# Kernel tuning notes

Hardware: AMD Instinct MI355X
Metric: run time of the kernel (lower is better)

## Reference

```python
import jax, jax.numpy as jnp
import numpy as np

HEADS = 20
HEAD_DIM = 64
NUM_IP = 20          # num_content_tokens (4) + num_style_tokens (16)
FU_SCALE = 0.5
STYLE_SCALE = 1.0
SCALE = 1.0 / np.sqrt(HEAD_DIM).astype(np.float32)


def setup_inputs() -> dict:
    key = jax.random.key(0)
    ks = jax.random.split(key, 9)
    B, S, H, C = 4, 4096, 1280, 2048
    T = 77 + NUM_IP  # text tokens + ip tokens
    w = 0.02
    return {
        "hidden_states": jax.random.normal(ks[0], (B, S, H), jnp.float32),
        "encoder_hidden_states": jax.random.normal(ks[1], (B, T, C), jnp.float32),
        "Wq": jax.random.normal(ks[2], (H, H), jnp.float32) * w,
        "Wk": jax.random.normal(ks[3], (H, C), jnp.float32) * w,
        "Wv": jax.random.normal(ks[4], (H, C), jnp.float32) * w,
        "Wk_ip": jax.random.normal(ks[5], (H, C), jnp.float32) * w,
        "Wv_ip": jax.random.normal(ks[6], (H, C), jnp.float32) * w,
        "Wo": jax.random.normal(ks[7], (H, H), jnp.float32) * w,
        "bo": jnp.zeros((H,), jnp.float32),
    }


def _to_heads(x):
    # [B, T, H] -> [B, heads, T, head_dim]
    B, T, _ = x.shape
    return x.reshape(B, T, HEADS, HEAD_DIM).transpose(0, 2, 1, 3)


def _blend(p):
    # cross-batch prob fusion: rows 1<-0, 3<-2 (CFG pairs)
    p = p.at[1].set(FU_SCALE * p[1] + (1.0 - FU_SCALE) * p[0])
    p = p.at[3].set(FU_SCALE * p[3] + (1.0 - FU_SCALE) * p[2])
    return p


def reference(hidden_states, encoder_hidden_states, Wq, Wk, Wv, Wk_ip, Wv_ip, Wo, bo):
    B, S, H = hidden_states.shape
    text = encoder_hidden_states[:, :-NUM_IP, :]   # [B, 77, C]
    ip = encoder_hidden_states[:, -NUM_IP:, :]     # [B, 20, C]

    q = _to_heads(hidden_states @ Wq.T)            # [B, h, S, d]
    k = _to_heads(text @ Wk.T)                     # [B, h, 77, d]
    v = _to_heads(text @ Wv.T)

    # fuAttn branch: explicit probs, blended across batch, then PV matmul
    probs = jax.nn.softmax(jnp.einsum('bhqd,bhkd->bhqk', q, k) * SCALE, axis=-1)
    probs = _blend(probs)
    raw = jnp.einsum('bhqk,bhkd->bhqd', probs, v)
    raw = raw.transpose(0, 2, 1, 3).reshape(B, S, H)

    # IP-adapter style cross-attention (fuIPAttn branch)
    ip_k = _to_heads(ip @ Wk_ip.T)                 # [B, h, 20, d]
    ip_v = _to_heads(ip @ Wv_ip.T)
    ip_probs = jax.nn.softmax(jnp.einsum('bhqd,bhkd->bhqk', q, ip_k) * SCALE, axis=-1)
    ip_probs = _blend(ip_probs)
    ip_hs = jnp.einsum('bhqk,bhkd->bhqd', ip_probs, ip_v)
    ip_hs = ip_hs.transpose(0, 2, 1, 3).reshape(B, S, H)

    hs = raw + STYLE_SCALE * ip_hs
    # batch rows 0 and 2 keep raw (text-only) attention output
    hs = hs.at[0].set(raw[0]).at[2].set(raw[2])

    # to_out[0] linear (bias) + to_out[1] dropout (identity at inference)
    return hs @ Wo.T + bo
```

## Files before the change

kernel.cpp:

```cpp
#include <hip/hip_runtime.h>
#include <cstdint>

typedef float floatx4 __attribute__((ext_vector_type(4)));
typedef __bf16 bf16x8 __attribute__((ext_vector_type(8)));

typedef const __attribute__((address_space(1))) void* gas_cvp;
typedef __attribute__((address_space(3))) void* las_vp;

__device__ __forceinline__ float bflo(unsigned int u) {
    return __builtin_bit_cast(float, u << 16);
}
__device__ __forceinline__ float bfhi(unsigned int u) {
    return __builtin_bit_cast(float, u & 0xffff0000u);
}
__device__ __forceinline__ unsigned short f2bf(float f) {
    unsigned int u = __builtin_bit_cast(unsigned int, f);
    u += 0x7fffu + ((u >> 16) & 1u);
    return (unsigned short)(u >> 16);
}
__device__ __forceinline__ bf16x8 ld8(const unsigned short* p) {
    return __builtin_bit_cast(bf16x8, *(const uint4*)p);
}
__device__ __forceinline__ floatx4 mfma32(bf16x8 a, bf16x8 b, floatx4 c) {
    return __builtin_amdgcn_mfma_f32_16x16x32_bf16(a, b, c, 0, 0, 0);
}
__device__ __forceinline__ void load_lds16(const void* g, void* l) {
    __builtin_amdgcn_global_load_lds(
        (gas_cvp)(unsigned long long)g,
        (las_vp)(unsigned int)(unsigned long long)l,
        16, 0, 0);
}

__global__ void cvt_f32_bf16(const float* __restrict__ in,
                             unsigned short* __restrict__ out, int n4) {
    int i = blockIdx.x * 256 + threadIdx.x;
    if (i < n4) {
        float4 v = ((const float4*)in)[i];
        ushort4 o;
        o.x = f2bf(v.x); o.y = f2bf(v.y); o.z = f2bf(v.z); o.w = f2bf(v.w);
        ((ushort4*)out)[i] = o;
    }
}

struct CvtJob { const float* src; unsigned short* dst; int n4; };
struct CvtJobs { CvtJob j[7]; };

__global__ void cvt_multi(CvtJobs jobs) {
    CvtJob jb = jobs.j[blockIdx.y];
    int i = blockIdx.x * 256 + threadIdx.x;
    if (i < jb.n4) {
        float4 v = ((const float4*)jb.src)[i];
        ushort4 o;
        o.x = f2bf(v.x); o.y = f2bf(v.y); o.z = f2bf(v.z); o.w = f2bf(v.w);
        ((ushort4*)jb.dst)[i] = o;
    }
}

struct GemmJob {
    const unsigned short* A;
    const unsigned short* B;
    void* C;
    int M, N, K;
    int rpb, bstride, roff;
};
struct GemmArgs { GemmJob j[5]; };

template <bool F32OUT>
__global__ __launch_bounds__(256, 2) void gemm_bt(GemmArgs args,
                                                  const float* __restrict__ bias) {
    GemmJob jb = args.j[blockIdx.z];
    const int ntiles = jb.N >> 7;
    const int mtiles = (jb.M + 127) >> 7;

    int bx, by;
    {
        int idx = blockIdx.x;
        if ((mtiles & 7) == 0) {
            int gsz = ntiles * 8;
            int group = idx / gsz;
            int rem = idx - group * gsz;
            by = group * 8 + (rem & 7);
            bx = rem >> 3;
        } else {
            by = idx / ntiles;
            bx = idx - by * ntiles;
        }
    }
    if (by * 128 >= jb.M) return;

    const int tid  = threadIdx.x;
    const int lane = tid & 63;
    const int wid  = tid >> 6;
    const int K = jb.K, N = jb.N;

    __shared__ unsigned short ldsA[128 * 32];
    __shared__ unsigned short ldsB[128 * 32];

    const int colA = (((tid & 3) ^ ((tid >> 3) & 3)) * 8);
    auto maprow = [&](int r) -> size_t {
        r = (r < jb.M) ? r : (jb.M - 1);
        int b = r / jb.rpb;
        int t = r - b * jb.rpb;
        return (size_t)(b * jb.bstride + jb.roff + t);
    };
    const unsigned short* pa0 = jb.A + maprow(by * 128 + (tid >> 2)) * K + colA;
    const unsigned short* pa1 = jb.A + maprow(by * 128 + 64 + (tid >> 2)) * K + colA;
    const unsigned short* pb0 = jb.B + (size_t)(bx * 128 + (tid >> 2)) * K + colA;
    const unsigned short* pb1 = jb.B + (size_t)(bx * 128 + 64 + (tid >> 2)) * K + colA;

    unsigned short* la0 = &ldsA[tid * 8];
    unsigned short* la1 = &ldsA[2048 + tid * 8];
    unsigned short* lb0 = &ldsB[tid * 8];
    unsigned short* lb1 = &ldsB[2048 + tid * 8];

    floatx4 acc[4][4] = {};

    const int wm = (wid & 1) * 64;
    const int wn = (wid >> 1) * 64;
    const int fr = lane & 15;
    const int g  = lane >> 4;
    const int fcs = (g ^ ((fr >> 1) & 3)) * 8;

    for (int k0 = 0; k0 < K; k0 += 32) {
        __syncthreads();
        load_lds16(pa0 + k0, la0);
        load_lds16(pa1 + k0, la1);
        load_lds16(pb0 + k0, lb0);
        load_lds16(pb1 + k0, lb1);
        __syncthreads();

        bf16x8 af[4], bfv[4];
#pragma unroll
        for (int i = 0; i < 4; i++)
            af[i] = *(const bf16x8*)&ldsA[(wm + i * 16 + fr) * 32 + fcs];
#pragma unroll
        for (int i = 0; i < 4; i++)
            bfv[i] = *(const bf16x8*)&ldsB[(wn + i * 16 + fr) * 32 + fcs];
#pragma unroll
        for (int mi = 0; mi < 4; mi++)
#pragma unroll
            for (int ni = 0; ni < 4; ni++)
                acc[mi][ni] = __builtin_amdgcn_mfma_f32_16x16x32_bf16(
                    af[mi], bfv[ni], acc[mi][ni], 0, 0, 0);
    }

    const int colBase = bx * 128 + wn;
    const int rowBase = by * 128 + wm;
#pragma unroll
    for (int mi = 0; mi < 4; mi++) {
#pragma unroll
        for (int ni = 0; ni < 4; ni++) {
            int col  = colBase + ni * 16 + fr;
            int row0 = rowBase + mi * 16 + g * 4;
#pragma unroll
            for (int r = 0; r < 4; r++) {
                int row = row0 + r;
                if (row < jb.M) {
                    float v = acc[mi][ni][r];
                    if (F32OUT)
                        ((float*)jb.C)[(size_t)row * N + col] = v + bias[col];
                    else
                        ((unsigned short*)jb.C)[(size_t)row * N + col] = f2bf(v);
                }
            }
        }
    }
}

#define NT 77
#define NI 20
#define VSTR 104
#define ISTR 40

__global__ __launch_bounds__(256, 2) void attn_mfma(
    const unsigned short* __restrict__ q,
    const unsigned short* __restrict__ kt,
    const unsigned short* __restrict__ vt,
    const unsigned short* __restrict__ kip,
    const unsigned short* __restrict__ vip,
    unsigned short* __restrict__ outp)
{
    const int tid = threadIdx.x;
    const int qt = blockIdx.x;
    const int h  = blockIdx.y;
    const int pz = blockIdx.z;
    const int b0 = 2 * pz;
    const int lane  = tid & 63;
    const int w     = tid >> 6;
    const int bi    = w >> 1;
    const int strip = (w & 1) * 16;
    const int fr = lane & 15;
    const int g  = lane >> 4;

    __shared__ unsigned short sVt[2][64][VSTR];
    __shared__ unsigned short sVipt[2][64][ISTR];
    __shared__ unsigned short sP[2][32][VSTR];

    for (int i = tid; i < 2 * 64 * (VSTR - NT); i += 256) {
        int b = i / (64 * (VSTR - NT)); int rem = i % (64 * (VSTR - NT));
        sVt[b][rem / (VSTR - NT)][NT + rem % (VSTR - NT)] = 0;
    }
    for (int i = tid; i < 2 * 64 * (ISTR - NI); i += 256) {
        int b = i / (64 * (ISTR - NI)); int rem = i % (64 * (ISTR - NI));
        sVipt[b][rem / (ISTR - NI)][NI + rem % (ISTR - NI)] = 0;
    }
    for (int i = tid; i < 2 * 32 * (VSTR - 80); i += 256) {
        int b = i / (32 * (VSTR - 80)); int rem = i % (32 * (VSTR - 80));
        sP[b][rem / (VSTR - 80)][80 + rem % (VSTR - 80)] = 0;
    }

    for (int c = tid; c < 2 * 8 * NT; c += 256) {
        int b = c / (8 * NT); int rem = c % (8 * NT);
        int dc = rem / NT; int key = rem % NT;
        uint4 v = *(const uint4*)&vt[((size_t)((b0 + b) * NT + key)) * 1280 + h * 64 + dc * 8];
        unsigned int uu[4] = {v.x, v.y, v.z, v.w};
#pragma unroll
        for (int j = 0; j < 4; j++) {
            sVt[b][dc * 8 + 2 * j][key]     = (unsigned short)(uu[j] & 0xffffu);
            sVt[b][dc * 8 + 2 * j + 1][key] = (unsigned short)(uu[j] >> 16);
        }
    }
    for (int c = tid; c < 2 * 8 * NI; c += 256) {
        int b = c / (8 * NI); int rem = c % (8 * NI);
        int dc = rem / NI; int key = rem % NI;
        uint4 v = *(const uint4*)&vip[((size_t)((b0 + b) * NI + key)) * 1280 + h * 64 + dc * 8];
        unsigned int uu[4] = {v.x, v.y, v.z, v.w};
#pragma unroll
        for (int j = 0; j < 4; j++) {
            sVipt[b][dc * 8 + 2 * j][key]     = (unsigned short)(uu[j] & 0xffffu);
            sVipt[b][dc * 8 + 2 * j + 1][key] = (unsigned short)(uu[j] >> 16);
        }
    }

    const size_t qbase = ((size_t)((b0 + bi) * 4096 + qt * 32 + strip + fr)) * 1280 + h * 64;
    bf16x8 aq0 = ld8(&q[qbase + g * 8]);
    bf16x8 aq1 = ld8(&q[qbase + 32 + g * 8]);

    floatx4 sc[5] = {};
#pragma unroll
    for (int t = 0; t < 5; t++) {
        int key = t * 16 + fr; key = (key < NT) ? key : (NT - 1);
        const size_t kb = ((size_t)((b0 + bi) * NT + key)) * 1280 + h * 64;
        sc[t] = mfma32(aq0, ld8(&kt[kb + g * 8]), sc[t]);
        sc[t] = mfma32(aq1, ld8(&kt[kb + 32 + g * 8]), sc[t]);
    }

#pragma unroll
    for (int r = 0; r < 4; r++) {
        float m = -1e30f;
#pragma unroll
        for (int t = 0; t < 5; t++) {
            float v = sc[t][r] * 0.125f;
            if (t == 4 && fr >= 13) v = -1e30f;
            sc[t][r] = v;
            m = fmaxf(m, v);
        }
        m = fmaxf(m, __shfl_xor(m, 1));
        m = fmaxf(m, __shfl_xor(m, 2));
        m = fmaxf(m, __shfl_xor(m, 4));
        m = fmaxf(m, __shfl_xor(m, 8));
        float sum = 0.f;
#pragma unroll
        for (int t = 0; t < 5; t++) {
            float e = __expf(sc[t][r] - m);
            sc[t][r] = e;
            sum += e;
        }
        sum += __shfl_xor(sum, 1);
        sum += __shfl_xor(sum, 2);
        sum += __shfl_xor(sum, 4);
        sum += __shfl_xor(sum, 8);
        float inv = 1.f / sum;
#pragma unroll
        for (int t = 0; t < 5; t++)
            sP[bi][strip + g * 4 + r][t * 16 + fr] = f2bf(sc[t][r] * inv);
    }
    __syncthreads();

    {
        unsigned int* p0 = (unsigned int*)&sP[0][0][0];
        unsigned int* p1 = (unsigned int*)&sP[1][0][0];
        for (int i = tid; i < 32 * VSTR / 2; i += 256) {
            unsigned int a = p0[i], b = p1[i];
            unsigned short r0 = f2bf(0.5f * (bflo(a) + bflo(b)));
            unsigned short r1 = f2bf(0.5f * (bfhi(a) + bfhi(b)));
            p1[i] = (unsigned int)r0 | ((unsigned int)r1 << 16);
        }
    }
    __syncthreads();

    floatx4 accO[4] = {};
    {
        const unsigned short* prow = &sP[bi][strip + fr][0];
        bf16x8 pa0 = ld8(prow + g * 8);
        bf16x8 pa1 = ld8(prow + 32 + g * 8);
        bf16x8 pa2 = ld8(prow + 64 + g * 8);
#pragma unroll
        for (int dt = 0; dt < 4; dt++) {
            const unsigned short* vrow = &sVt[bi][dt * 16 + fr][0];
            accO[dt] = mfma32(pa0, ld8(vrow + g * 8), accO[dt]);
            accO[dt] = mfma32(pa1, ld8(vrow + 32 + g * 8), accO[dt]);
            accO[dt] = mfma32(pa2, ld8(vrow + 64 + g * 8), accO[dt]);
        }
    }

    floatx4 si[2] = {};
#pragma unroll
    for (int t = 0; t < 2; t++) {
        int key = t * 16 + fr; key = (key < NI) ? key : (NI - 1);
        const size_t kb = ((size_t)((b0 + bi) * NI + key)) * 1280 + h * 64;
        si[t] = mfma32(aq0, ld8(&kip[kb + g * 8]), si[t]);
        si[t] = mfma32(aq1, ld8(&kip[kb + 32 + g * 8]), si[t]);
    }
#pragma unroll
    for (int r = 0; r < 4; r++) {
        float v0 = si[0][r] * 0.125f;
        float v1 = (fr >= 4) ? -1e30f : si[1][r] * 0.125f;
        float m = fmaxf(v0, v1);
        m = fmaxf(m, __shfl_xor(m, 1));
        m = fmaxf(m, __shfl_xor(m, 2));
        m = fmaxf(m, __shfl_xor(m, 4));
        m = fmaxf(m, __shfl_xor(m, 8));
        float e0 = __expf(v0 - m), e1 = __expf(v1 - m);
        float s = e0 + e1;
        s += __shfl_xor(s, 1);
        s += __shfl_xor(s, 2);
        s += __shfl_xor(s, 4);
        s += __shfl_xor(s, 8);
        float inv = 1.f / s;
        si[0][r] = e0 * inv;
        si[1][r] = e1 * inv;
    }
    __syncthreads();

#pragma unroll
    for (int r = 0; r < 4; r++) {
        sP[bi][strip + g * 4 + r][fr]      = f2bf(si[0][r]);
        sP[bi][strip + g * 4 + r][16 + fr] = f2bf(si[1][r]);
    }
    __syncthreads();

    for (int i = tid; i < 32 * 16; i += 256) {
        int r = i >> 4, kk = i & 15;
        unsigned int* p0 = (unsigned int*)&sP[0][r][0];
        unsigned int* p1 = (unsigned int*)&sP[1][r][0];
        unsigned int a = p0[kk], b = p1[kk];
        unsigned short r0 = f2bf(0.5f * (bflo(a) + bflo(b)));
        unsigned short r1 = f2bf(0.5f * (bfhi(a) + bfhi(b)));
        p1[kk] = (unsigned int)r0 | ((unsigned int)r1 << 16);
    }
    __syncthreads();

    if (bi == 1) {
        const unsigned short* prow = &sP[1][strip + fr][0];
        bf16x8 pip = ld8(prow + g * 8);
#pragma unroll
        for (int dt = 0; dt < 4; dt++)
            accO[dt] = mfma32(pip, ld8(&sVipt[1][dt * 16 + fr][g * 8]), accO[dt]);
    }

    const size_t orow0 = (size_t)((b0 + bi) * 4096 + qt * 32 + strip);
#pragma unroll
    for (int dt = 0; dt < 4; dt++) {
        int col = h * 64 + dt * 16 + fr;
#pragma unroll
        for (int r = 0; r < 4; r++)
            outp[(orow0 + g * 4 + r) * 1280 + col] = f2bf(accO[dt][r]);
    }
}

extern "C" void kernel_launch(void* const* d_in, const int* in_sizes, int n_in,
                              void* d_out, int out_size, void* d_ws, size_t ws_size,
                              hipStream_t stream) {
    const float* hs   = (const float*)d_in[0];
    const float* ehs  = (const float*)d_in[1];
    const float* Wq   = (const float*)d_in[2];
    const float* Wk   = (const float*)d_in[3];
    const float* Wv   = (const float*)d_in[4];
    const float* Wkip = (const float*)d_in[5];
    const float* Wvip = (const float*)d_in[6];
    const float* Wo   = (const float*)d_in[7];
    const float* bo   = (const float*)d_in[8];

    char* w = (char*)d_ws;
    size_t off = 0;
    auto alloc = [&](size_t bytes) {
        char* pp = w + off;
        off += (bytes + 255) & ~(size_t)255;
        return pp;
    };
    unsigned short* hs_bf   = (unsigned short*)alloc(16384ull * 1280 * 2);
    unsigned short* q_bf    = (unsigned short*)alloc(16384ull * 1280 * 2);
    unsigned short* at_bf   = (unsigned short*)alloc(16384ull * 1280 * 2);
    unsigned short* ehs_bf  = (unsigned short*)alloc(4ull * 97 * 2048 * 2);
    unsigned short* Wq_bf   = (unsigned short*)alloc(1280ull * 1280 * 2);
    unsigned short* Wk_bf   = (unsigned short*)alloc(1280ull * 2048 * 2);
    unsigned short* Wv_bf   = (unsigned short*)alloc(1280ull * 2048 * 2);
    unsigned short* Wkip_bf = (unsigned short*)alloc(1280ull * 2048 * 2);
    unsigned short* Wvip_bf = (unsigned short*)alloc(1280ull * 2048 * 2);
    unsigned short* Wo_bf   = (unsigned short*)alloc(1280ull * 1280 * 2);
    unsigned short* kt  = (unsigned short*)alloc(308ull * 1280 * 2);
    unsigned short* vt  = (unsigned short*)alloc(308ull * 1280 * 2);
    unsigned short* kip = (unsigned short*)alloc(80ull * 1280 * 2);
    unsigned short* vip = (unsigned short*)alloc(80ull * 1280 * 2);

    cvt_f32_bf16<<<dim3(20480, 1, 1), 256, 0, stream>>>(hs, hs_bf, 16384 * 1280 / 4);

    CvtJobs cj{};
    cj.j[0] = CvtJob{ehs,  ehs_bf,  (int)(4ull * 97 * 2048 / 4)};
    cj.j[1] = CvtJob{Wq,   Wq_bf,   1280 * 1280 / 4};
    cj.j[2] = CvtJob{Wk,   Wk_bf,   1280 * 2048 / 4};
    cj.j[3] = CvtJob{Wv,   Wv_bf,   1280 * 2048 / 4};
    cj.j[4] = CvtJob{Wkip, Wkip_bf, 1280 * 2048 / 4};
    cj.j[5] = CvtJob{Wvip, Wvip_bf, 1280 * 2048 / 4};
    cj.j[6] = CvtJob{Wo,   Wo_bf,   1280 * 1280 / 4};
    cvt_multi<<<dim3(2560, 7, 1), 256, 0, stream>>>(cj);

    GemmArgs gq{};
    gq.j[0] = GemmJob{hs_bf,  Wq_bf,   (void*)q_bf, 16384, 1280, 1280, 16384, 0, 0};
    gq.j[1] = GemmJob{ehs_bf, Wk_bf,   (void*)kt,     308, 1280, 2048, 77, 97, 0};
    gq.j[2] = GemmJob{ehs_bf, Wv_bf,   (void*)vt,     308, 1280, 2048, 77, 97, 0};
    gq.j[3] = GemmJob{ehs_bf, Wkip_bf, (void*)kip,     80, 1280, 2048, 20, 97, 77};
    gq.j[4] = GemmJob{ehs_bf, Wvip_bf, (void*)vip,     80, 1280, 2048, 20, 97, 77};
    gemm_bt<false><<<dim3(1280, 1, 5), 256, 0, stream>>>(gq, nullptr);

    attn_mfma<<<dim3(128, 20, 2), 256, 0, stream>>>(q_bf, kt, vt, kip, vip, at_bf);

    GemmArgs go{};
    go.j[0] = GemmJob{at_bf, Wo_bf, d_out, 16384, 1280, 1280, 16384, 0, 0};
    gemm_bt<true><<<dim3(1280, 1, 1), 256, 0, stream>>>(go, bo);
}
```

Baseline: 453.4 us.

## Replace GEMM with 256x256-tile double-buffered pipelined kernel and flattened job grid

Rewrites the bf16 GEMM from 128x128 tiles with 256 threads and a single-stage LDS buffer into a 256x256-tile, 512-thread kernel. It uses a double-buffered 64-deep K loop that interleaves global-to-LDS prefetch with four MFMA phases, adds s_setprio and explicit vmcnt waits, and uses a swizzled LDS layout. The per-job launch with z-dimension and early exit is replaced by a flat block list with per-job start offsets, so the small K/V projections and the Q projection share one grid without idle blocks. The goal is higher MFMA utilization and more reuse per loaded byte. In exchange, N is hardcoded to 1280, LDS use is larger (128 KB per block), and the small-M jobs waste more of each 256-row tile.

```diff
diff --git a/kernel.cpp b/kernel.cpp
--- a/kernel.cpp
+++ b/kernel.cpp
@@ -56,111 +56,194 @@
     }
 }
 
-struct GemmJob {
+struct GJob {
     const unsigned short* A;
     const unsigned short* B;
     void* C;
-    int M, N, K;
+    int M, K;
     int rpb, bstride, roff;
+    int bstart;
 };
-struct GemmArgs { GemmJob j[5]; };
+struct GArgs { GJob j[5]; };
+
+#define GBAR() do { __builtin_amdgcn_s_barrier(); __builtin_amdgcn_sched_barrier(0); } while (0)
 
 template <bool F32OUT>
-__global__ __launch_bounds__(256, 2) void gemm_bt(GemmArgs args,
+__global__ __launch_bounds__(512, 2) void gemm256(GArgs args,
                                                   const float* __restrict__ bias) {
-    GemmJob jb = args.j[blockIdx.z];
-    const int ntiles = jb.N >> 7;
-    const int mtiles = (jb.M + 127) >> 7;
-
-    int bx, by;
+    const int tid = threadIdx.x;
+    int jid = 0;
+#pragma unroll
+    for (int t = 1; t < 5; ++t)
+        if ((int)blockIdx.x >= args.j[t].bstart) jid = t;
+    const GJob jb = args.j[jid];
+    const int K = jb.K;
+    int b = (int)blockIdx.x - jb.bstart;
     {
-        int idx = blockIdx.x;
-        if ((mtiles & 7) == 0) {
-            int gsz = ntiles * 8;
-            int group = idx / gsz;
-            int rem = idx - group * gsz;
-            by = group * 8 + (rem & 7);
-            bx = rem >> 3;
-        } else {
-            by = idx / ntiles;
-            bx = idx - by * ntiles;
-        }
-    }
-    if (by * 128 >= jb.M) return;
-
-    const int tid  = threadIdx.x;
-    const int lane = tid & 63;
-    const int wid  = tid >> 6;
-    const int K = jb.K, N = jb.N;
-
-    __shared__ unsigned short ldsA[128 * 32];
-    __shared__ unsigned short ldsB[128 * 32];
-
-    const int colA = (((tid & 3) ^ ((tid >> 3) & 3)) * 8);
+        const int mt = (jb.M + 255) >> 8;
+        const int nblk = mt * 5;
+        if ((nblk & 7) == 0) b = (b & 7) * (nblk >> 3) + (b >> 3);
+    }
+    const int by = b / 5, bx = b - by * 5;
+
+    __shared__ unsigned short ldsA[32768];
+    __shared__ unsigned short ldsB[32768];
+
+    const int srow   = ((tid >> 7) << 4) + ((tid >> 2) & 15);
+    const int schunk = ((tid & 3) << 4) ^ (((tid >> 2) & 6) << 3);
+    const int scol   = (((tid >> 6) & 1) << 5) + (schunk >> 1);
+
+    const int Mloc = jb.M, rpbL = jb.rpb, bstrL = jb.bstride, roffL = jb.roff;
     auto maprow = [&](int r) -> size_t {
-        r = (r < jb.M) ? r : (jb.M - 1);
-        int b = r / jb.rpb;
-        int t = r - b * jb.rpb;
-        return (size_t)(b * jb.bstride + jb.roff + t);
+        r = (r < Mloc) ? r : (Mloc - 1);
+        int blk = r / rpbL;
+        return (size_t)(blk * bstrL + roffL + (r - blk * rpbL));
     };
-    const unsigned short* pa0 = jb.A + maprow(by * 128 + (tid >> 2)) * K + colA;
-    const unsigned short* pa1 = jb.A + maprow(by * 128 + 64 + (tid >> 2)) * K + colA;
-    const unsigned short* pb0 = jb.B + (size_t)(bx * 128 + (tid >> 2)) * K + colA;
-    const unsigned short* pb1 = jb.B + (size_t)(bx * 128 + 64 + (tid >> 2)) * K + colA;
-
-    unsigned short* la0 = &ldsA[tid * 8];
-    unsigned short* la1 = &ldsA[2048 + tid * 8];
-    unsigned short* lb0 = &ldsB[tid * 8];
-    unsigned short* lb1 = &ldsB[2048 + tid * 8];
-
-    floatx4 acc[4][4] = {};
-
-    const int wm = (wid & 1) * 64;
-    const int wn = (wid >> 1) * 64;
-    const int fr = lane & 15;
-    const int g  = lane >> 4;
-    const int fcs = (g ^ ((fr >> 1) & 3)) * 8;
-
-    for (int k0 = 0; k0 < K; k0 += 32) {
-        __syncthreads();
-        load_lds16(pa0 + k0, la0);
-        load_lds16(pa1 + k0, la1);
-        load_lds16(pb0 + k0, lb0);
-        load_lds16(pb1 + k0, lb1);
-        __syncthreads();
-
-        bf16x8 af[4], bfv[4];
-#pragma unroll
-        for (int i = 0; i < 4; i++)
-            af[i] = *(const bf16x8*)&ldsA[(wm + i * 16 + fr) * 32 + fcs];
-#pragma unroll
-        for (int i = 0; i < 4; i++)
-            bfv[i] = *(const bf16x8*)&ldsB[(wn + i * 16 + fr) * 32 + fcs];
-#pragma unroll
-        for (int mi = 0; mi < 4; mi++)
-#pragma unroll
-            for (int ni = 0; ni < 4; ni++)
-                acc[mi][ni] = __builtin_amdgcn_mfma_f32_16x16x32_bf16(
-                    af[mi], bfv[ni], acc[mi][ni], 0, 0, 0);
-    }
-
-    const int colBase = bx * 128 + wn;
-    const int rowBase = by * 128 + wm;
-#pragma unroll
-    for (int mi = 0; mi < 4; mi++) {
-#pragma unroll
-        for (int ni = 0; ni < 4; ni++) {
-            int col  = colBase + ni * 16 + fr;
-            int row0 = rowBase + mi * 16 + g * 4;
-#pragma unroll
-            for (int r = 0; r < 4; r++) {
-                int row = row0 + r;
-                if (row < jb.M) {
-                    float v = acc[mi][ni][r];
+
+    const unsigned short* pA[2][2];
+    const unsigned short* pB[2][2];
+    unsigned short* dA[2][2];
+    unsigned short* dB[2][2];
+#pragma unroll
+    for (int h = 0; h < 2; ++h)
+#pragma unroll
+        for (int j = 0; j < 2; ++j) {
+            const int r = h * 128 + j * 64 + srow;
+            pA[h][j] = jb.A + maprow(by * 256 + r) * K + scol;
+            pB[h][j] = jb.B + (size_t)(bx * 256 + r) * K + scol;
+            dA[h][j] = &ldsA[h * 8192 + j * 4096 + tid * 8];
+            dB[h][j] = &ldsB[h * 8192 + j * 4096 + tid * 8];
+        }
+
+    const int lane = tid & 63, fr = lane & 15, g = lane >> 4;
+    const int w = tid >> 6, wr = w & 1, wc = w >> 1;
+    const int rb   = fr * 32 + ((g * 8) ^ ((fr & 6) << 2));
+    const int aoff = wr * 8192 + rb;
+    const int boff = (wc >> 1) * 8192 + (wc & 1) * 4096 + rb;
+
+    floatx4 acc[8][4] = {};
+    bf16x8 af[4][2], bn0[2][2], bn1[2][2];
+
+    const int KT = K >> 6;
+
+    load_lds16(pA[0][0], dA[0][0]); load_lds16(pA[0][1], dA[0][1]);
+    load_lds16(pA[1][0], dA[1][0]); load_lds16(pA[1][1], dA[1][1]);
+    load_lds16(pB[0][0], dB[0][0]); load_lds16(pB[0][1], dB[0][1]);
+    load_lds16(pB[1][0], dB[1][0]); load_lds16(pB[1][1], dB[1][1]);
+    load_lds16(pB[0][0] + 64, dB[0][0] + 16384);
+    load_lds16(pB[0][1] + 64, dB[0][1] + 16384);
+    load_lds16(pA[0][0] + 64, dA[0][0] + 16384);
+    load_lds16(pA[0][1] + 64, dA[0][1] + 16384);
+    asm volatile("s_waitcnt vmcnt(4)" ::: "memory");
+    GBAR();
+
+    for (int u = 0; u < KT; ++u) {
+        const int pb = (u & 1) << 14;
+        const int qb = pb ^ 16384;
+        const int k1 = (u + 1 < KT) ? (u + 1) : (KT - 1);
+        const int k2 = (u + 2 < KT) ? (u + 2) : (KT - 1);
+
+#pragma unroll
+        for (int mi = 0; mi < 4; ++mi)
+#pragma unroll
+            for (int kk = 0; kk < 2; ++kk)
+                af[mi][kk] = *(const bf16x8*)&ldsA[pb + aoff + (mi * 2 + kk) * 512];
+#pragma unroll
+        for (int nf = 0; nf < 2; ++nf)
+#pragma unroll
+            for (int kk = 0; kk < 2; ++kk)
+                bn0[nf][kk] = *(const bf16x8*)&ldsB[pb + boff + (nf * 2 + kk) * 512];
+        load_lds16(pA[1][0] + (size_t)k1 * 64, dA[1][0] + qb);
+        load_lds16(pA[1][1] + (size_t)k1 * 64, dA[1][1] + qb);
+        GBAR();
+        __builtin_amdgcn_s_setprio(1);
+#pragma unroll
+        for (int kk = 0; kk < 2; ++kk)
+#pragma unroll
+            for (int mi = 0; mi < 4; ++mi)
+#pragma unroll
+                for (int nf = 0; nf < 2; ++nf)
+                    acc[mi][nf] = mfma32(af[mi][kk], bn0[nf][kk], acc[mi][nf]);
+        __builtin_amdgcn_s_setprio(0);
+        GBAR();
+
+#pragma unroll
+        for (int nf = 0; nf < 2; ++nf)
+#pragma unroll
+            for (int kk = 0; kk < 2; ++kk)
+                bn1[nf][kk] = *(const bf16x8*)&ldsB[pb + boff + ((nf + 2) * 2 + kk) * 512];
+        load_lds16(pB[1][0] + (size_t)k1 * 64, dB[1][0] + qb);
+        load_lds16(pB[1][1] + (size_t)k1 * 64, dB[1][1] + qb);
+        GBAR();
+        __builtin_amdgcn_s_setprio(1);
+#pragma unroll
+        for (int kk = 0; kk < 2; ++kk)
+#pragma unroll
+            for (int mi = 0; mi < 4; ++mi)
+#pragma unroll
+                for (int nf = 0; nf < 2; ++nf)
+                    acc[mi][nf + 2] = mfma32(af[mi][kk], bn1[nf][kk], acc[mi][nf + 2]);
+        __builtin_amdgcn_s_setprio(0);
+        GBAR();
+
+#pragma unroll
+        for (int mi = 0; mi < 4; ++mi)
+#pragma unroll
+            for (int kk = 0; kk < 2; ++kk)
+                af[mi][kk] = *(const bf16x8*)&ldsA[pb + aoff + ((mi + 4) * 2 + kk) * 512];
+        load_lds16(pB[0][0] + (size_t)k2 * 64, dB[0][0] + pb);
+        load_lds16(pB[0][1] + (size_t)k2 * 64, dB[0][1] + pb);
+        GBAR();
+        __builtin_amdgcn_s_setprio(1);
+#pragma unroll
+        for (int kk = 0; kk < 2; ++kk)
+#pragma unroll
+            for (int mi = 0; mi < 4; ++mi)
+#pragma unroll
+                for (int nf = 0; nf < 2; ++nf)
+                    acc[mi + 4][nf + 2] = mfma32(af[mi][kk], bn1[nf][kk], acc[mi + 4][nf + 2]);
+        __builtin_amdgcn_s_setprio(0);
+        GBAR();
+
+        load_lds16(pA[0][0] + (size_t)k2 * 64, dA[0][0] + pb);
+        load_lds16(pA[0][1] + (size_t)k2 * 64, dA[0][1] + pb);
+        GBAR();
+        __builtin_amdgcn_s_setprio(1);
+#pragma unroll
+        for (int kk = 0; kk < 2; ++kk)
+#pragma unroll
+            for (int mi = 0; mi < 4; ++mi)
+#pragma unroll
+                for (int nf = 0; nf < 2; ++nf)
+                    acc[mi + 4][nf] = mfma32(af[mi][kk], bn0[nf][kk], acc[mi + 4][nf]);
+        __builtin_amdgcn_s_setprio(0);
+        asm volatile("s_waitcnt vmcnt(4)" ::: "memory");
+        GBAR();
+    }
+    asm volatile("s_waitcnt vmcnt(0)" ::: "memory");
+
+    const int colBase = bx * 256 + wc * 64;
+    const int rowBase = by * 256 + wr * 128;
+    float bv[4] = {};
+    if (F32OUT) {
+#pragma unroll
+        for (int nf = 0; nf < 4; ++nf) bv[nf] = bias[colBase + nf * 16 + fr];
+    }
+#pragma unroll
+    for (int mi = 0; mi < 8; ++mi) {
+#pragma unroll
+        for (int nf = 0; nf < 4; ++nf) {
+            const int col  = colBase + nf * 16 + fr;
+            const int row0 = rowBase + mi * 16 + g * 4;
+#pragma unroll
+            for (int r = 0; r < 4; ++r) {
+                const int row = row0 + r;
+                if (row < Mloc) {
+                    float v = acc[mi][nf][r];
                     if (F32OUT)
-                        ((float*)jb.C)[(size_t)row * N + col] = v + bias[col];
+                        ((float*)jb.C)[(size_t)row * 1280 + col] = v + bv[nf];
                     else
-                        ((unsigned short*)jb.C)[(size_t)row * N + col] = f2bf(v);
+                        ((unsigned short*)jb.C)[(size_t)row * 1280 + col] = f2bf(v);
                 }
             }
         }
@@ -416,17 +499,18 @@
     cj.j[6] = CvtJob{Wo,   Wo_bf,   1280 * 1280 / 4};
     cvt_multi<<<dim3(2560, 7, 1), 256, 0, stream>>>(cj);
 
-    GemmArgs gq{};
-    gq.j[0] = GemmJob{hs_bf,  Wq_bf,   (void*)q_bf, 16384, 1280, 1280, 16384, 0, 0};
-    gq.j[1] = GemmJob{ehs_bf, Wk_bf,   (void*)kt,     308, 1280, 2048, 77, 97, 0};
-    gq.j[2] = GemmJob{ehs_bf, Wv_bf,   (void*)vt,     308, 1280, 2048, 77, 97, 0};
-    gq.j[3] = GemmJob{ehs_bf, Wkip_bf, (void*)kip,     80, 1280, 2048, 20, 97, 77};
-    gq.j[4] = GemmJob{ehs_bf, Wvip_bf, (void*)vip,     80, 1280, 2048, 20, 97, 77};
-    gemm_bt<false><<<dim3(1280, 1, 5), 256, 0, stream>>>(gq, nullptr);
+    GArgs g1{};
+    g1.j[0] = GJob{ehs_bf, Wk_bf,   (void*)kt,    308, 2048,    77, 97,  0,  0};
+    g1.j[1] = GJob{ehs_bf, Wv_bf,   (void*)vt,    308, 2048,    77, 97,  0, 10};
+    g1.j[2] = GJob{ehs_bf, Wkip_bf, (void*)kip,    80, 2048,    20, 97, 77, 20};
+    g1.j[3] = GJob{ehs_bf, Wvip_bf, (void*)vip,    80, 2048,    20, 97, 77, 25};
+    g1.j[4] = GJob{hs_bf,  Wq_bf,   (void*)q_bf, 16384, 1280, 16384,  0,  0, 30};
+    gemm256<false><<<dim3(350, 1, 1), 512, 0, stream>>>(g1, nullptr);
 
     attn_mfma<<<dim3(128, 20, 2), 256, 0, stream>>>(q_bf, kt, vt, kip, vip, at_bf);
 
-    GemmArgs go{};
-    go.j[0] = GemmJob{at_bf, Wo_bf, d_out, 16384, 1280, 1280, 16384, 0, 0};
-    gemm_bt<true><<<dim3(1280, 1, 1), 256, 0, stream>>>(go, bo);
-}
+    GArgs g2{};
+    g2.j[0] = GJob{at_bf, Wo_bf, d_out, 16384, 1280, 16384, 0, 0, 0};
+    for (int t = 1; t < 5; ++t) g2.j[t].bstart = 0x7fffffff;
+    gemm256<true><<<dim3(320, 1, 1), 512, 0, stream>>>(g2, bo);
+}
```

New measurement: 442.8 us. -2.3%, faster.
